# Kernel tuning notes

Hardware: AMD Instinct MI355X
Metric: run time of the kernel (lower is better)

Reference implementation:

```python
import jax, jax.numpy as jnp
import numpy as np

E, H, M = 1024, 16, 256
B, S = 2, 2048
D = E // H
SCALE = D ** -0.5


def setup_inputs() -> dict:
    key = jax.random.key(0)
    ks = jax.random.split(key, 10)
    p = 0.02
    return {
        "x": jax.random.normal(ks[0], (B, S, E), jnp.float32),
        "Wq": jax.random.normal(ks[1], (E, E), jnp.float32) * p,
        "bq": jax.random.normal(ks[2], (E,), jnp.float32) * p,
        "Wk": jax.random.normal(ks[3], (E, E), jnp.float32) * p,
        "bk": jax.random.normal(ks[4], (E,), jnp.float32) * p,
        "Wv": jax.random.normal(ks[5], (E, E), jnp.float32) * p,
        "bv": jax.random.normal(ks[6], (E,), jnp.float32) * p,
        "Wo": jax.random.normal(ks[7], (E, E), jnp.float32) * p,
        "bo": jax.random.normal(ks[8], (E,), jnp.float32) * p,
        "memory_state": jax.random.normal(ks[9], (M, E), jnp.float32) * p,
    }


def reference(x, Wq, bq, Wk, bk, Wv, bv, Wo, bo, memory_state):
    b, s, e = x.shape
    # QKV projections (torch Linear: y = x W^T + b), split heads -> [b,h,s,d]
    q = (x @ Wq.T + bq).reshape(b, s, H, D).transpose(0, 2, 1, 3)
    k = (x @ Wk.T + bk).reshape(b, s, H, D).transpose(0, 2, 1, 3)
    v = (x @ Wv.T + bv).reshape(b, s, H, D).transpose(0, 2, 1, 3)
    # full self-attention (eval mode: dropout is identity)
    attn = jax.nn.softmax(jnp.einsum("bhqd,bhkd->bhqk", q, k) * SCALE, axis=-1)
    attn_out = jnp.einsum("bhqk,bhkd->bhqd", attn, v)
    attn_out = attn_out.transpose(0, 2, 1, 3).reshape(b, s, e)
    # memory-read cross-attention on raw x against compressed memory [M,E]
    mem_w = jax.nn.softmax(jnp.einsum("bse,me->bsm", x, memory_state) * SCALE, axis=-1)
    mem_out = jnp.einsum("bsm,me->bse", mem_w, memory_state)
    out = attn_out + 0.5 * mem_out
    return out @ Wo.T + bo
```

## Files before the change

### kernel.cpp

```cpp
#include <hip/hip_runtime.h>
#include <cstdint>
#include <cstddef>


typedef __bf16 bf16;
typedef bf16  bf16x8 __attribute__((ext_vector_type(8)));
typedef bf16  bf16x4 __attribute__((ext_vector_type(4)));
typedef float f32x4  __attribute__((ext_vector_type(4)));
typedef float f32x16 __attribute__((ext_vector_type(16)));
typedef int   i32x4  __attribute__((ext_vector_type(4)));
typedef int   i32x2  __attribute__((ext_vector_type(2)));

#define B_DIM 2
#define S_DIM 2048
#define E_DIM 1024
#define H_DIM 16
#define D_DIM 64
#define M_DIM 256
#define NROW  (B_DIM * S_DIM)
#define C1 0.18033688011112042f

#define MFMA32(a, b, c) __builtin_amdgcn_mfma_f32_32x32x16_bf16((a), (b), (c), 0, 0, 0)

__device__ __forceinline__ f32x16 zero16()
{
    f32x16 z;
#pragma unroll
    for (int i = 0; i < 16; ++i) z[i] = 0.f;
    return z;
}

__device__ __forceinline__ void async_cp16(const bf16* g, bf16* l)
{
    __builtin_amdgcn_global_load_lds(
        (const __attribute__((address_space(1))) void*)g,
        (__attribute__((address_space(3))) void*)l, 16, 0, 0);
}

__global__ void __launch_bounds__(256)
conv_all(const float* __restrict__ x,  const float* __restrict__ Wq,
         const float* __restrict__ Wk, const float* __restrict__ Wv,
         const float* __restrict__ Wo, const float* __restrict__ mem,
         bf16* __restrict__ xb,  bf16* __restrict__ Wqb,
         bf16* __restrict__ Wkb, bf16* __restrict__ Wvb,
         bf16* __restrict__ Wob, bf16* __restrict__ memb,
         bf16* __restrict__ memt)
{
    int t = blockIdx.x * 256 + threadIdx.x;
    const float* src; bf16* dst; int off; bool is_mem = false;
    if      (t <  524288) { src = x;   dst = xb;   off = t; }
    else if (t <  655360) { src = Wq;  dst = Wqb;  off = t - 524288; }
    else if (t <  786432) { src = Wk;  dst = Wkb;  off = t - 655360; }
    else if (t <  917504) { src = Wv;  dst = Wvb;  off = t - 786432; }
    else if (t < 1048576) { src = Wo;  dst = Wob;  off = t - 917504; }
    else                  { src = mem; dst = memb; off = t - 1048576; is_mem = true; }
    const float4* p = (const float4*)src + (size_t)off * 2;
    float4 a = p[0], b = p[1];
    bf16x8 o;
    o[0] = (bf16)a.x; o[1] = (bf16)a.y; o[2] = (bf16)a.z; o[3] = (bf16)a.w;
    o[4] = (bf16)b.x; o[5] = (bf16)b.y; o[6] = (bf16)b.z; o[7] = (bf16)b.w;
    *(bf16x8*)(dst + (size_t)off * 8) = o;
    if (is_mem) {
        int r = off >> 7, c0 = (off & 127) * 8;
        float h[8] = {a.x, a.y, a.z, a.w, b.x, b.y, b.z, b.w};
#pragma unroll
        for (int j = 0; j < 8; ++j)
            memt[(size_t)(c0 + j) * M_DIM + r] = (bf16)(0.5f * h[j]);
    }
}

struct GemmAcc { f32x4 a[4][4]; };

__device__ __forceinline__ void
gemm_core(const bf16* __restrict__ A, const bf16* __restrict__ Bm,
          int K, int m0, int n0, bf16* As, bf16* Bs, GemmAcc& R)
{
    const int tid  = threadIdx.x;
    const int lane = tid & 63;
    const int wave = tid >> 6;
    const int quad = lane >> 4;
    const int l16  = lane & 15;
    const int wm   = (wave >> 1) * 64;
    const int wn   = (wave & 1) * 64;

#pragma unroll
    for (int i = 0; i < 4; ++i)
#pragma unroll
        for (int j = 0; j < 4; ++j)
            R.a[i][j] = f32x4{0.f, 0.f, 0.f, 0.f};

    int s_c0  = wave * 128 + lane;
    int s_r0  = s_c0 >> 2;
    int s_k0  = (s_c0 & 3) ^ ((s_r0 >> 1) & 3);
    int s_c1  = s_c0 + 64;
    int s_r1  = s_c1 >> 2;
    int s_k1  = (s_c1 & 3) ^ ((s_r1 >> 1) & 3);
    const bf16* gA0 = A  + (size_t)(m0 + s_r0) * K + s_k0 * 8;
    const bf16* gA1 = A  + (size_t)(m0 + s_r1) * K + s_k1 * 8;
    const bf16* gB0 = Bm + (size_t)(n0 + s_r0) * K + s_k0 * 8;
    const bf16* gB1 = Bm + (size_t)(n0 + s_r1) * K + s_k1 * 8;

#define STAGE(buf, k0)                                                     \
    do {                                                                   \
        async_cp16(gA0 + (k0), &As[(buf) * 4096 + wave * 1024]);           \
        async_cp16(gA1 + (k0), &As[(buf) * 4096 + wave * 1024 + 512]);     \
        async_cp16(gB0 + (k0), &Bs[(buf) * 4096 + wave * 1024]);           \
        async_cp16(gB1 + (k0), &Bs[(buf) * 4096 + wave * 1024 + 512]);     \
    } while (0)

    STAGE(0, 0);
    int buf = 0;
    for (int k0 = 0; k0 < K; k0 += 32) {
        __syncthreads();
        if (k0 + 32 < K) STAGE(buf ^ 1, k0 + 32);

        const bf16* Ab = As + buf * 4096;
        const bf16* Bb = Bs + buf * 4096;
        bf16x8 af[4], bfr[4];
#pragma unroll
        for (int mi = 0; mi < 4; ++mi) {
            int m    = wm + mi * 16 + l16;
            int slot = quad ^ ((m >> 1) & 3);
            af[mi]   = *(const bf16x8*)(&Ab[(m * 4 + slot) * 8]);
        }
#pragma unroll
        for (int ni = 0; ni < 4; ++ni) {
            int n    = wn + ni * 16 + l16;
            int slot = quad ^ ((n >> 1) & 3);
            bfr[ni]  = *(const bf16x8*)(&Bb[(n * 4 + slot) * 8]);
        }
#pragma unroll
        for (int mi = 0; mi < 4; ++mi)
#pragma unroll
            for (int ni = 0; ni < 4; ++ni)
                R.a[mi][ni] = __builtin_amdgcn_mfma_f32_16x16x32_bf16(
                    af[mi], bfr[ni], R.a[mi][ni], 0, 0, 0);
        buf ^= 1;
    }
#undef STAGE
}

__global__ void __launch_bounds__(256, 3)
gemm_qkvl(const bf16* __restrict__ A,
          const bf16* __restrict__ Wq, const bf16* __restrict__ Wk,
          const bf16* __restrict__ Wv, const bf16* __restrict__ memb,
          const float* __restrict__ bq, const float* __restrict__ bk,
          const float* __restrict__ bv,
          bf16* __restrict__ q, bf16* __restrict__ k,
          bf16* __restrict__ vt, bf16* __restrict__ lg)
{
    __shared__ __align__(16) bf16 As[2 * 4096];
    __shared__ __align__(16) bf16 Bs[2 * 4096];
    const int lid  = blockIdx.x;
    const int xcd  = lid & 7;
    const int idx  = lid >> 3;
    const int mloc = idx / 26;
    const int nn   = idx - mloc * 26;
    const int m0   = (mloc * 8 + xcd) * 128;
    const int widx = (nn < 24) ? (nn >> 3) : 3;
    const int n0   = (nn < 24) ? (nn & 7) * 128 : (nn - 24) * 128;
    const bf16*  Bm = (widx == 0) ? Wq : (widx == 1) ? Wk :
                      (widx == 2) ? Wv : memb;
    GemmAcc R;
    gemm_core(A, Bm, E_DIM, m0, n0, As, Bs, R);

    const int lane = threadIdx.x & 63, wave = threadIdx.x >> 6;
    const int quad = lane >> 4, l16 = lane & 15;
    const int wm = (wave >> 1) * 64, wn = (wave & 1) * 64;

    if (widx == 0 || widx == 1) {
        bf16* C = (widx == 0) ? q : k;
        const float* bi = (widx == 0) ? bq : bk;
        float scale = (widx == 0) ? C1 : 1.0f;
#pragma unroll
        for (int ni = 0; ni < 4; ++ni) {
            int col  = n0 + wn + ni * 16 + l16;
            float bb = bi[col];
#pragma unroll
            for (int mi = 0; mi < 4; ++mi)
#pragma unroll
                for (int r = 0; r < 4; ++r) {
                    int rowg = m0 + wm + mi * 16 + quad * 4 + r;
                    C[(size_t)rowg * E_DIM + col] =
                        (bf16)((R.a[mi][ni][r] + bb) * scale);
                }
        }
    } else if (widx == 2) {
#pragma unroll
        for (int ni = 0; ni < 4; ++ni) {
            int col = n0 + wn + ni * 16 + l16;
            float bb = bv[col];
#pragma unroll
            for (int mi = 0; mi < 4; ++mi) {
                int row0 = m0 + wm + mi * 16 + quad * 4;
                int bidx = row0 >> 11, s = row0 & 2047;
                bf16x4 pk;
#pragma unroll
                for (int r = 0; r < 4; ++r) pk[r] = (bf16)(R.a[mi][ni][r] + bb);
                *(bf16x4*)(&vt[((size_t)(bidx * H_DIM) * 64 + col) * S_DIM + s]) = pk;
            }
        }
    } else {
#pragma unroll
        for (int ni = 0; ni < 4; ++ni) {
            int col = n0 + wn + ni * 16 + l16;
#pragma unroll
            for (int mi = 0; mi < 4; ++mi)
#pragma unroll
                for (int r = 0; r < 4; ++r) {
                    int rowg = m0 + wm + mi * 16 + quad * 4 + r;
                    lg[(size_t)rowg * M_DIM + col] = (bf16)R.a[mi][ni][r];
                }
        }
    }
}

__global__ void __launch_bounds__(256, 2)
gemm_out64(const bf16* __restrict__ A, const bf16* __restrict__ Bm,
           const float* __restrict__ bias, float* __restrict__ C)
{
    __shared__ __align__(16) bf16 As[2 * 2048];
    __shared__ __align__(16) bf16 Bs[2 * 4096];
    const int tid  = threadIdx.x;
    const int lane = tid & 63;
    const int wave = tid >> 6;
    const int quad = lane >> 4;
    const int l16  = lane & 15;
    const int wm   = (wave >> 1) * 32;
    const int wn   = (wave & 1) * 64;
    const int lid  = blockIdx.x;
    const int xcd  = lid & 7;
    const int idx  = lid >> 3;
    const int mloc = idx >> 3;
    const int nn   = idx & 7;
    const int m0   = (mloc * 8 + xcd) * 64;
    const int n0   = nn * 128;
    const int K    = E_DIM;

    f32x4 acc[2][4];
#pragma unroll
    for (int i = 0; i < 2; ++i)
#pragma unroll
        for (int j = 0; j < 4; ++j) acc[i][j] = f32x4{0.f, 0.f, 0.f, 0.f};

    int a_s  = wave * 64 + lane;
    int a_r  = a_s >> 2;
    int a_k  = (a_s & 3) ^ ((a_r >> 1) & 3);
    int b_s0 = wave * 128 + lane;
    int b_r0 = b_s0 >> 2;
    int b_k0 = (b_s0 & 3) ^ ((b_r0 >> 1) & 3);
    int b_s1 = b_s0 + 64;
    int b_r1 = b_s1 >> 2;
    int b_k1 = (b_s1 & 3) ^ ((b_r1 >> 1) & 3);
    const bf16* gA  = A  + (size_t)(m0 + a_r) * K + a_k * 8;
    const bf16* gB0 = Bm + (size_t)(n0 + b_r0) * K + b_k0 * 8;
    const bf16* gB1 = Bm + (size_t)(n0 + b_r1) * K + b_k1 * 8;

#define STAGE64(buf, k0)                                                   \
    do {                                                                   \
        async_cp16(gA  + (k0), &As[(buf) * 2048 + wave * 512]);            \
        async_cp16(gB0 + (k0), &Bs[(buf) * 4096 + wave * 1024]);           \
        async_cp16(gB1 + (k0), &Bs[(buf) * 4096 + wave * 1024 + 512]);     \
    } while (0)

    STAGE64(0, 0);
    int buf = 0;
    for (int k0 = 0; k0 < K; k0 += 32) {
        __syncthreads();
        if (k0 + 32 < K) STAGE64(buf ^ 1, k0 + 32);
        const bf16* Ab = As + buf * 2048;
        const bf16* Bb = Bs + buf * 4096;
        bf16x8 af[2], bfr[4];
#pragma unroll
        for (int mi = 0; mi < 2; ++mi) {
            int m    = wm + mi * 16 + l16;
            int slot = quad ^ ((m >> 1) & 3);
            af[mi]   = *(const bf16x8*)(&Ab[(m * 4 + slot) * 8]);
        }
#pragma unroll
        for (int ni = 0; ni < 4; ++ni) {
            int n    = wn + ni * 16 + l16;
            int slot = quad ^ ((n >> 1) & 3);
            bfr[ni]  = *(const bf16x8*)(&Bb[(n * 4 + slot) * 8]);
        }
#pragma unroll
        for (int mi = 0; mi < 2; ++mi)
#pragma unroll
            for (int ni = 0; ni < 4; ++ni)
                acc[mi][ni] = __builtin_amdgcn_mfma_f32_16x16x32_bf16(
                    af[mi], bfr[ni], acc[mi][ni], 0, 0, 0);
        buf ^= 1;
    }
#undef STAGE64

#pragma unroll
    for (int ni = 0; ni < 4; ++ni) {
        int col  = n0 + wn + ni * 16 + l16;
        float bb = bias[col];
#pragma unroll
        for (int mi = 0; mi < 2; ++mi)
#pragma unroll
            for (int r = 0; r < 4; ++r) {
                int rowg = m0 + wm + mi * 16 + quad * 4 + r;
                C[(size_t)rowg * E_DIM + col] = acc[mi][ni][r] + bb;
            }
    }
}

__global__ void __launch_bounds__(256, 4)
flash_attn(const bf16* __restrict__ q, const bf16* __restrict__ k,
           const bf16* __restrict__ vt, const bf16* __restrict__ lg,
           const bf16* __restrict__ memt, bf16* __restrict__ outc)
{
    __shared__ __align__(16) bf16 SM[16384];
    const int tid  = threadIdx.x;
    const int lane = tid & 63;
    const int wave = tid >> 6;
    const int hi   = lane >> 5;
    const int l32  = lane & 31;
    const int pw   = wave & 1;
    const int ks   = wave >> 1;

    const int lid = blockIdx.x;
    const int xcd = lid & 7;
    const int kk  = lid >> 3;
    const int qt  = kk & 31;
    const int p   = ((kk >> 5) << 3) | xcd;
    const int b   = p >> 4;
    const int h   = p & 15;
    const int q0  = qt * 64;
    const int qw  = q0 + pw * 32;

    const bf16* qb = q  + (size_t)(b * S_DIM + qw) * E_DIM + h * D_DIM;
    const bf16* kb = k  + (size_t)(b * S_DIM) * E_DIM + h * D_DIM;
    const bf16* vb = vt + (size_t)(b * H_DIM + h) * D_DIM * S_DIM;
    const int   kv0 = ks * 1024;

    bf16* Kb0 = SM + ks * 8192;
    bf16* Vb0 = SM + ks * 8192 + 4096;

    const int pl = pw * 64 + lane;
    const int kr0 = pl >> 3;
    const int kg0 = (pl & 7) ^ (kr0 & 7);
    const bf16* gK0 = kb + (size_t)(kv0 + kr0) * E_DIM + kg0 * 8;
    const bf16* gK1 = gK0 + (size_t)16 * E_DIM;
    const int kd0 = pl * 8;
    const int vd0 = pl >> 2;
    const int vg0 = (pl & 3) ^ (vd0 & 3);
    const bf16* gV0 = vb + (size_t)vd0 * S_DIM + kv0 + vg0 * 8;
    const bf16* gV1 = gV0 + (size_t)32 * S_DIM;
    const int v00 = vd0 * 32 + (((vg0 & ~1)    ) ^ (vd0 & 3)) * 8 + (vg0 & 1) * 4;
    const int v01 = vd0 * 32 + (((vg0 & ~1) | 1) ^ (vd0 & 3)) * 8 + (vg0 & 1) * 4;

    bf16x8 qfr[4];
#pragma unroll
    for (int c = 0; c < 4; ++c)
        qfr[c] = *(const bf16x8*)(qb + (size_t)l32 * E_DIM + c * 16 + hi * 8);

    bf16x8 vones;
#pragma unroll
    for (int j = 0; j < 8; ++j) vones[j] = (bf16)1.0f;

    f32x16 o0 = zero16(), o1 = zero16(), osum = zero16();

    {
        i32x4 rK0 = *(const i32x4*)(gK0);
        i32x4 rK1 = *(const i32x4*)(gK1);
        i32x4 rV0 = *(const i32x4*)(gV0);
        i32x4 rV1 = *(const i32x4*)(gV1);
        *(i32x4*)(Kb0 + kd0)        = rK0;
        *(i32x4*)(Kb0 + kd0 + 1024) = rK1;
        *(i32x2*)(Vb0 + v00)        = i32x2{rV0[0], rV0[1]};
        *(i32x2*)(Vb0 + v01)        = i32x2{rV0[2], rV0[3]};
        *(i32x2*)(Vb0 + v00 + 1024) = i32x2{rV1[0], rV1[1]};
        *(i32x2*)(Vb0 + v01 + 1024) = i32x2{rV1[2], rV1[3]};
    }
    __syncthreads();

    int buf = 0;
    for (int kt = 0; kt < 1024; kt += 32) {
        const bool pre = (kt + 32 < 1024);
        i32x4 nK0, nK1, nV0, nV1;
        if (pre) {
            const size_t ko = (size_t)(kt + 32) * E_DIM;
            nK0 = *(const i32x4*)(gK0 + ko);
            nK1 = *(const i32x4*)(gK1 + ko);
            nV0 = *(const i32x4*)(gV0 + (kt + 32));
            nV1 = *(const i32x4*)(gV1 + (kt + 32));
        }
        const bf16* Kb = Kb0 + buf * 2048;
        const bf16* Vb = Vb0 + buf * 2048;

        f32x16 sc0 = zero16();
        __builtin_amdgcn_s_setprio(1);
#pragma unroll
        for (int c = 0; c < 4; ++c) {
            const int swz = ((c * 2 + hi) ^ (l32 & 7)) * 8;
            bf16x8 kf = *(const bf16x8*)(&Kb[l32 * 64 + swz]);
            sc0 = MFMA32(kf, qfr[c], sc0);
        }
        __builtin_amdgcn_s_setprio(0);

        bf16x8 ap[2];
#pragma unroll
        for (int kc = 0; kc < 2; ++kc)
#pragma unroll
            for (int j = 0; j < 8; ++j)
                ap[kc][j] = (bf16)exp2f(sc0[kc * 8 + j]);

        __builtin_amdgcn_s_setprio(1);
#pragma unroll
        for (int kc = 0; kc < 2; ++kc) {
            const int swz = ((kc * 2 + hi) ^ (l32 & 3)) * 8;
            bf16x8 vf0 = *(const bf16x8*)(&Vb[l32 * 32 + swz]);
            bf16x8 vf1 = *(const bf16x8*)(&Vb[(32 + l32) * 32 + swz]);
            o0   = MFMA32(ap[kc], vf0, o0);
            o1   = MFMA32(ap[kc], vf1, o1);
            osum = MFMA32(ap[kc], vones, osum);
        }
        __builtin_amdgcn_s_setprio(0);

        if (pre) {
            const int bo = (buf ^ 1) * 2048;
            *(i32x4*)(Kb0 + bo + kd0)        = nK0;
            *(i32x4*)(Kb0 + bo + kd0 + 1024) = nK1;
            *(i32x2*)(Vb0 + bo + v00)        = i32x2{nV0[0], nV0[1]};
            *(i32x2*)(Vb0 + bo + v01)        = i32x2{nV0[2], nV0[3]};
            *(i32x2*)(Vb0 + bo + v00 + 1024) = i32x2{nV1[0], nV1[1]};
            *(i32x2*)(Vb0 + bo + v01 + 1024) = i32x2{nV1[2], nV1[3]};
        }
        __syncthreads();
        buf ^= 1;
    }

    float* smf = (float*)SM;
    if (ks == 1) {
        float* dst = smf + pw * 3072 + lane;
#pragma unroll
        for (int i = 0; i < 16; ++i) dst[i * 64]        = o0[i];
#pragma unroll
        for (int i = 0; i < 16; ++i) dst[(16 + i) * 64] = o1[i];
#pragma unroll
        for (int i = 0; i < 16; ++i) dst[(32 + i) * 64] = osum[i];
    }
    __syncthreads();
    if (ks == 1) return;
    {
        const float* src = smf + pw * 3072 + lane;
#pragma unroll
        for (int i = 0; i < 16; ++i) o0[i]   += src[i * 64];
#pragma unroll
        for (int i = 0; i < 16; ++i) o1[i]   += src[(16 + i) * 64];
#pragma unroll
        for (int i = 0; i < 16; ++i) osum[i] += src[(32 + i) * 64];
    }

    float linv[16];
#pragma unroll
    for (int r = 0; r < 16; ++r) linv[r] = 1.f / osum[r];

    const bf16* Pr = lg   + (size_t)(b * S_DIM + qw) * M_DIM;
    const bf16* Mt = memt + (size_t)(h * D_DIM) * M_DIM;
    f32x16 macc0 = zero16(), macc1 = zero16(), msum = zero16();
#pragma unroll
    for (int mc = 0; mc < 16; ++mc) {
        bf16x8 raw = *(const bf16x8*)(Pr + (size_t)l32 * M_DIM + mc * 16 + hi * 8);
        bf16x8 epv;
#pragma unroll
        for (int j = 0; j < 8; ++j) epv[j] = (bf16)exp2f(C1 * (float)raw[j]);
        bf16x8 bm0 = *(const bf16x8*)(Mt + (size_t)l32 * M_DIM        + mc * 16 + hi * 8);
        bf16x8 bm1 = *(const bf16x8*)(Mt + (size_t)(32 + l32) * M_DIM + mc * 16 + hi * 8);
        macc0 = MFMA32(epv, bm0, macc0);
        macc1 = MFMA32(epv, bm1, macc1);
        msum  = MFMA32(epv, vones, msum);
    }

    bf16* ob = outc + (size_t)(b * S_DIM + qw) * E_DIM + h * D_DIM;
#pragma unroll
    for (int r = 0; r < 16; ++r) {
        const int qrow = (r & 3) + 8 * (r >> 2) + 4 * hi;
        const float mi = 1.f / msum[r];
        ob[(size_t)qrow * E_DIM + l32]      = (bf16)(o0[r] * linv[r] + macc0[r] * mi);
        ob[(size_t)qrow * E_DIM + 32 + l32] = (bf16)(o1[r] * linv[r] + macc1[r] * mi);
    }
}

extern "C" void kernel_launch(void* const* d_in, const int* in_sizes, int n_in,
                              void* d_out, int out_size, void* d_ws, size_t ws_size,
                              hipStream_t stream)
{
    (void)in_sizes; (void)n_in; (void)out_size; (void)ws_size;
    const float* x   = (const float*)d_in[0];
    const float* Wq  = (const float*)d_in[1];
    const float* bq  = (const float*)d_in[2];
    const float* Wk  = (const float*)d_in[3];
    const float* bk  = (const float*)d_in[4];
    const float* Wv  = (const float*)d_in[5];
    const float* bv  = (const float*)d_in[6];
    const float* Wo  = (const float*)d_in[7];
    const float* bo  = (const float*)d_in[8];
    const float* mem = (const float*)d_in[9];
    float* out = (float*)d_out;

    bf16* w = (bf16*)d_ws;
    const size_t NE = (size_t)NROW * E_DIM;
    const size_t EE = (size_t)E_DIM * E_DIM;
    bf16* xb      = w;
    bf16* q_ws    = w + NE;
    bf16* k_ws    = w + 2 * NE;
    bf16* Wqb     = w + 3 * NE;
    bf16* Wkb     = Wqb + EE;
    bf16* Wvb     = Wkb + EE;
    bf16* Wob     = Wvb + EE;
    bf16* memb    = Wob + EE;
    bf16* lg_ws   = memb + (size_t)M_DIM * E_DIM;
    bf16* memt_ws = lg_ws + (size_t)NROW * M_DIM;
    bf16* vt_ws = (bf16*)d_out;

    dim3 blk(256);

    conv_all<<<dim3(4224), blk, 0, stream>>>(
        x, Wq, Wk, Wv, Wo, mem, xb, Wqb, Wkb, Wvb, Wob, memb, memt_ws);

    gemm_qkvl<<<dim3(832), blk, 0, stream>>>(
        xb, Wqb, Wkb, Wvb, memb, bq, bk, bv, q_ws, k_ws, vt_ws, lg_ws);

    flash_attn<<<dim3(1024), blk, 0, stream>>>(
        q_ws, k_ws, vt_ws, lg_ws, memt_ws, q_ws);

    gemm_out64<<<dim3(512), blk, 0, stream>>>(
        q_ws, Wob, bo, out);
}
```

Before: 224.3 us.

## Use single-buffered 64-key tiles in flash attention with split prefetch

The attention inner loop now handles 64 keys per iteration instead of 32, in a single LDS buffer rather than a double buffer. V is loaded with a 64-wide row layout and an XOR swizzle. The global prefetch for V is delayed until after the QK MFMAs to spread register pressure, and the launch-bounds occupancy hint drops from 4 to 3 blocks. The aim is fewer loop iterations and barriers per unit of work and more MFMA work between syncs. The cost is an extra barrier per iteration, because there is no double buffer, plus more registers and possibly lower occupancy.

```diff
diff --git a/kernel.cpp b/kernel.cpp
--- a/kernel.cpp
+++ b/kernel.cpp
@@ -307,7 +307,7 @@
     }
 }
 
-__global__ void __launch_bounds__(256, 4)
+__global__ void __launch_bounds__(256, 3)
 flash_attn(const bf16* __restrict__ q, const bf16* __restrict__ k,
            const bf16* __restrict__ vt, const bf16* __restrict__ lg,
            const bf16* __restrict__ memt, bf16* __restrict__ outc)
@@ -328,29 +328,24 @@
     const int p   = ((kk >> 5) << 3) | xcd;
     const int b   = p >> 4;
     const int h   = p & 15;
-    const int q0  = qt * 64;
-    const int qw  = q0 + pw * 32;
+    const int qw  = qt * 64 + pw * 32;
 
     const bf16* qb = q  + (size_t)(b * S_DIM + qw) * E_DIM + h * D_DIM;
     const bf16* kb = k  + (size_t)(b * S_DIM) * E_DIM + h * D_DIM;
     const bf16* vb = vt + (size_t)(b * H_DIM + h) * D_DIM * S_DIM;
     const int   kv0 = ks * 1024;
 
-    bf16* Kb0 = SM + ks * 8192;
-    bf16* Vb0 = SM + ks * 8192 + 4096;
-
-    const int pl = pw * 64 + lane;
-    const int kr0 = pl >> 3;
-    const int kg0 = (pl & 7) ^ (kr0 & 7);
-    const bf16* gK0 = kb + (size_t)(kv0 + kr0) * E_DIM + kg0 * 8;
-    const bf16* gK1 = gK0 + (size_t)16 * E_DIM;
-    const int kd0 = pl * 8;
-    const int vd0 = pl >> 2;
-    const int vg0 = (pl & 3) ^ (vd0 & 3);
-    const bf16* gV0 = vb + (size_t)vd0 * S_DIM + kv0 + vg0 * 8;
-    const bf16* gV1 = gV0 + (size_t)32 * S_DIM;
-    const int v00 = vd0 * 32 + (((vg0 & ~1)    ) ^ (vd0 & 3)) * 8 + (vg0 & 1) * 4;
-    const int v01 = vd0 * 32 + (((vg0 & ~1) | 1) ^ (vd0 & 3)) * 8 + (vg0 & 1) * 4;
+    bf16* Kp = SM + ks * 8192;
+    bf16* Vp = SM + ks * 8192 + 4096;
+
+    const int pl  = pw * 64 + lane;
+    const int r0  = pl >> 3;
+    const int g0  = (pl & 7) ^ (r0 & 7);
+    const bf16* gK = kb + (size_t)(kv0 + r0) * E_DIM + g0 * 8;
+    const bf16* gV = vb + (size_t)r0 * S_DIM + kv0 + g0 * 8;
+    const int kd  = pl * 8;
+    const int va  = r0 * 64 + (((g0 & ~1)    ) ^ (r0 & 7)) * 8 + (g0 & 1) * 4;
+    const int vb2 = r0 * 64 + (((g0 & ~1) | 1) ^ (r0 & 7)) * 8 + (g0 & 1) * 4;
 
     bf16x8 qfr[4];
 #pragma unroll
@@ -364,73 +359,82 @@
     f32x16 o0 = zero16(), o1 = zero16(), osum = zero16();
 
     {
-        i32x4 rK0 = *(const i32x4*)(gK0);
-        i32x4 rK1 = *(const i32x4*)(gK1);
-        i32x4 rV0 = *(const i32x4*)(gV0);
-        i32x4 rV1 = *(const i32x4*)(gV1);
-        *(i32x4*)(Kb0 + kd0)        = rK0;
-        *(i32x4*)(Kb0 + kd0 + 1024) = rK1;
-        *(i32x2*)(Vb0 + v00)        = i32x2{rV0[0], rV0[1]};
-        *(i32x2*)(Vb0 + v01)        = i32x2{rV0[2], rV0[3]};
-        *(i32x2*)(Vb0 + v00 + 1024) = i32x2{rV1[0], rV1[1]};
-        *(i32x2*)(Vb0 + v01 + 1024) = i32x2{rV1[2], rV1[3]};
+        i32x4 rk[4], rv[4];
+#pragma unroll
+        for (int i = 0; i < 4; ++i) rk[i] = *(const i32x4*)(gK + (size_t)(16 * i) * E_DIM);
+#pragma unroll
+        for (int i = 0; i < 4; ++i) rv[i] = *(const i32x4*)(gV + (size_t)(16 * i) * S_DIM);
+#pragma unroll
+        for (int i = 0; i < 4; ++i) *(i32x4*)(Kp + kd + i * 1024) = rk[i];
+#pragma unroll
+        for (int i = 0; i < 4; ++i) {
+            *(i32x2*)(Vp + va  + i * 1024) = i32x2{rv[i][0], rv[i][1]};
+            *(i32x2*)(Vp + vb2 + i * 1024) = i32x2{rv[i][2], rv[i][3]};
+        }
     }
     __syncthreads();
 
-    int buf = 0;
-    for (int kt = 0; kt < 1024; kt += 32) {
-        const bool pre = (kt + 32 < 1024);
-        i32x4 nK0, nK1, nV0, nV1;
+    for (int kt = 0; kt < 1024; kt += 64) {
+        const bool pre = (kt + 64 < 1024);
+        i32x4 nk[4], nv[4];
         if (pre) {
-            const size_t ko = (size_t)(kt + 32) * E_DIM;
-            nK0 = *(const i32x4*)(gK0 + ko);
-            nK1 = *(const i32x4*)(gK1 + ko);
-            nV0 = *(const i32x4*)(gV0 + (kt + 32));
-            nV1 = *(const i32x4*)(gV1 + (kt + 32));
-        }
-        const bf16* Kb = Kb0 + buf * 2048;
-        const bf16* Vb = Vb0 + buf * 2048;
-
-        f32x16 sc0 = zero16();
+            const size_t ko = (size_t)(kt + 64) * E_DIM;
+#pragma unroll
+            for (int i = 0; i < 4; ++i)
+                nk[i] = *(const i32x4*)(gK + ko + (size_t)(16 * i) * E_DIM);
+        }
+
+        f32x16 sc0 = zero16(), sc1 = zero16();
         __builtin_amdgcn_s_setprio(1);
 #pragma unroll
         for (int c = 0; c < 4; ++c) {
             const int swz = ((c * 2 + hi) ^ (l32 & 7)) * 8;
-            bf16x8 kf = *(const bf16x8*)(&Kb[l32 * 64 + swz]);
-            sc0 = MFMA32(kf, qfr[c], sc0);
+            bf16x8 kf0 = *(const bf16x8*)(&Kp[l32 * 64 + swz]);
+            bf16x8 kf1 = *(const bf16x8*)(&Kp[(32 + l32) * 64 + swz]);
+            sc0 = MFMA32(kf0, qfr[c], sc0);
+            sc1 = MFMA32(kf1, qfr[c], sc1);
         }
         __builtin_amdgcn_s_setprio(0);
 
-        bf16x8 ap[2];
-#pragma unroll
-        for (int kc = 0; kc < 2; ++kc)
+        if (pre) {
+#pragma unroll
+            for (int i = 0; i < 4; ++i)
+                nv[i] = *(const i32x4*)(gV + (kt + 64) + (size_t)(16 * i) * S_DIM);
+        }
+
+        bf16x8 ap[4];
+#pragma unroll
+        for (int kc = 0; kc < 4; ++kc) {
+            const f32x16 sct = (kc < 2) ? sc0 : sc1;
+            const int base = (kc & 1) * 8;
 #pragma unroll
             for (int j = 0; j < 8; ++j)
-                ap[kc][j] = (bf16)exp2f(sc0[kc * 8 + j]);
+                ap[kc][j] = (bf16)exp2f(sct[base + j]);
+        }
 
         __builtin_amdgcn_s_setprio(1);
 #pragma unroll
-        for (int kc = 0; kc < 2; ++kc) {
-            const int swz = ((kc * 2 + hi) ^ (l32 & 3)) * 8;
-            bf16x8 vf0 = *(const bf16x8*)(&Vb[l32 * 32 + swz]);
-            bf16x8 vf1 = *(const bf16x8*)(&Vb[(32 + l32) * 32 + swz]);
+        for (int kc = 0; kc < 4; ++kc) {
+            const int swz = ((kc * 2 + hi) ^ (l32 & 7)) * 8;
+            bf16x8 vf0 = *(const bf16x8*)(&Vp[l32 * 64 + swz]);
+            bf16x8 vf1 = *(const bf16x8*)(&Vp[(32 + l32) * 64 + swz]);
             o0   = MFMA32(ap[kc], vf0, o0);
             o1   = MFMA32(ap[kc], vf1, o1);
             osum = MFMA32(ap[kc], vones, osum);
         }
         __builtin_amdgcn_s_setprio(0);
 
+        __syncthreads();
         if (pre) {
-            const int bo = (buf ^ 1) * 2048;
-            *(i32x4*)(Kb0 + bo + kd0)        = nK0;
-            *(i32x4*)(Kb0 + bo + kd0 + 1024) = nK1;
-            *(i32x2*)(Vb0 + bo + v00)        = i32x2{nV0[0], nV0[1]};
-            *(i32x2*)(Vb0 + bo + v01)        = i32x2{nV0[2], nV0[3]};
-            *(i32x2*)(Vb0 + bo + v00 + 1024) = i32x2{nV1[0], nV1[1]};
-            *(i32x2*)(Vb0 + bo + v01 + 1024) = i32x2{nV1[2], nV1[3]};
+#pragma unroll
+            for (int i = 0; i < 4; ++i) *(i32x4*)(Kp + kd + i * 1024) = nk[i];
+#pragma unroll
+            for (int i = 0; i < 4; ++i) {
+                *(i32x2*)(Vp + va  + i * 1024) = i32x2{nv[i][0], nv[i][1]};
+                *(i32x2*)(Vp + vb2 + i * 1024) = i32x2{nv[i][2], nv[i][3]};
+            }
         }
         __syncthreads();
-        buf ^= 1;
     }
 
     float* smf = (float*)SM;
```

Measured after the change: 224.6 us. Within noise of the previous version (+0.1%).
